# Kernel optimization log

Hardware: AMD Instinct MI355X
Metric: run time of the kernel (lower is better)

Reference implementation:

```python
import jax, jax.numpy as jnp
import numpy as np

COMMITMENT_COST = 0.25


def setup_inputs() -> dict:
    key = jax.random.key(0)
    k1, k2 = jax.random.split(key)
    x = jax.random.normal(k1, (32, 256, 32, 32), dtype=jnp.float32)
    codebook = jax.random.normal(k2, (1024, 256), dtype=jnp.float32) * 0.02
    return {"x": x, "codebook": codebook}


def reference(x, codebook):
    # x: [B, C, H, W] -> z: [B, H, W, C] (NHWC), C = embedding_dim
    B, C, H, W = x.shape
    z = jnp.transpose(x, (0, 2, 3, 1))
    zf = z.reshape(-1, C)  # [N, C], N = B*H*W
    # squared euclidean distance: ||z||^2 - 2 z.e + ||e||^2  -> [N, K]
    d = (
        jnp.sum(zf * zf, axis=-1, keepdims=True)
        - 2.0 * (zf @ codebook.T)
        + jnp.sum(codebook * codebook, axis=-1)
    )
    encoding_indices = jnp.argmin(d, axis=1)  # [N]
    quantized = codebook[encoding_indices].reshape(z.shape)  # [B, H, W, C]

    # training losses (entropy_loss_ratio == 0 -> entropy branch skipped)
    sg = jax.lax.stop_gradient
    e_latent_loss = jnp.mean((sg(quantized) - z) ** 2) * COMMITMENT_COST
    q_latent_loss = jnp.mean((quantized - sg(z)) ** 2)
    quantizer_loss = e_latent_loss + q_latent_loss

    # straight-through estimator
    quantized_st = z + sg(quantized - z)
    out = jnp.transpose(quantized_st, (0, 3, 1, 2))  # back to NCHW
    return out, quantizer_loss, e_latent_loss, q_latent_loss, encoding_indices
```

## Files before the change

### kernel.cpp

```cpp
#include <hip/hip_runtime.h>
#include <cfloat>

#define C_DIM   256
#define HW      1024
#define N_ROWS  32768
#define K_CODES 1024
#define ROWS    64
#define NCHUNK  32
#define WCHUNK_BYTES 8192
#define LISTCAP 128
#define DELTA   0.008f

#define OUT_ELEMS 8388608
#define LOSS_OFF  8388608
#define IDX_OFF   8388611

typedef _Float16 half8 __attribute__((ext_vector_type(8)));
typedef _Float16 f16x4 __attribute__((ext_vector_type(4)));
typedef float    f32x4 __attribute__((ext_vector_type(4)));

#define AS1 __attribute__((address_space(1)))
#define AS3 __attribute__((address_space(3)))

#define OFF_EBUF  0
#define OFF_EN    65536
#define OFF_S32   69632
#define OFF_M1W   69888
#define OFF_THR   70400
#define OFF_RES   70656
#define OFF_FIDX  71168
#define OFF_LCNT  71424
#define OFF_LMETA 71680
#define SMEM_BYTES 73728

#define QT_STRIDE 258

#define DPP_MIN(x, ctrl) fminf((x), __int_as_float(__builtin_amdgcn_update_dpp(0, __float_as_int(x), (ctrl), 0xf, 0xf, true)))

__global__ void prep_kernel(const float* __restrict__ cb, float* __restrict__ enorm,
                            char* __restrict__ cb16) {
    int k = blockIdx.x * 4 + (threadIdx.x >> 6);
    int lane = threadIdx.x & 63;
    float4 v = *(const float4*)(cb + k * C_DIM + lane * 4);
    double s = (double)v.x * v.x + (double)v.y * v.y + (double)v.z * v.z + (double)v.w * v.w;
    #pragma unroll
    for (int m = 1; m < 64; m <<= 1) s += __shfl_xor(s, m, 64);
    if (lane == 0) enorm[k] = (float)s;
    f16x4 h;
    h[0] = (_Float16)v.x; h[1] = (_Float16)v.y; h[2] = (_Float16)v.z; h[3] = (_Float16)v.w;
    int dst = ((k >> 5) << 14) + ((k & 31) << 9)
            + ((lane * 8) ^ ((k & 15) << 4) ^ ((k & 1) << 8));
    *(f16x4*)(cb16 + dst) = h;
}

__global__ __launch_bounds__(256, 2) void vq_main(
    const float* __restrict__ x, const float* __restrict__ cb,
    const float* __restrict__ enorm_g, const char* __restrict__ cb16,
    float* __restrict__ out, float* __restrict__ idx_out, float* __restrict__ t2_out)
{
    extern __shared__ char smem[];
    float* qt      = (float*)(smem + OFF_EBUF);
    float* en_lds  = (float*)(smem + OFF_EN);
    float* S32     = (float*)(smem + OFF_S32);
    float* m1w     = (float*)(smem + OFF_M1W);
    float* thr     = (float*)(smem + OFF_THR);
    unsigned long long* res = (unsigned long long*)(smem + OFF_RES);
    int*   fidx    = (int*)(smem + OFF_FIDX);
    int*   lcnt    = (int*)(smem + OFF_LCNT);
    unsigned int* lmeta = (unsigned int*)(smem + OFF_LMETA);

    const int t    = threadIdx.x;
    const int lane = t & 63;
    const int wv   = t >> 6;
    const int wr   = wv >> 1;
    const int wc   = wv & 1;
    const int l15  = lane & 15;
    const int l4   = lane >> 4;
    const int row0 = blockIdx.x * ROWS;
    const int b    = row0 >> 10;
    const int hw0  = row0 & 1023;
    const float* xb = x + b * (C_DIM * HW) + hw0;

    char* ebw = smem + OFF_EBUF + wv * (2 * WCHUNK_BYTES);
    const char* cbw = cb16 + (wc << 13);

    #pragma unroll
    for (int c2 = 0; c2 < 2; c2++) {
        const char* src = cbw + (c2 << 14);
        char* dst = ebw + c2 * WCHUNK_BYTES;
        #pragma unroll
        for (int i = 0; i < 8; i++) {
            __builtin_amdgcn_global_load_lds((const AS1 unsigned int*)(src + i * 1024 + lane * 16),
                                             (AS3 unsigned int*)(dst + i * 1024), 16, 0, 0);
        }
    }

    *(float4*)&en_lds[t * 4] = *(const float4*)(enorm_g + t * 4);
    if (t < 4) lcnt[t] = 0;

    half8 af[2][8];
    double s64[2] = {0.0, 0.0};
    #pragma unroll
    for (int rt = 0; rt < 2; rt++) {
        const float* xr = xb + wr * 32 + rt * 16 + l15;
        #pragma unroll
        for (int kk = 0; kk < 8; kk++) {
            float v[8];
            #pragma unroll
            for (int j = 0; j < 8; j++) v[j] = xr[(kk * 32 + l4 * 8 + j) * HW];
            #pragma unroll
            for (int j = 0; j < 8; j++) s64[rt] = fma((double)v[j], (double)v[j], s64[rt]);
            half8 h;
            #pragma unroll
            for (int j = 0; j < 8; j++) h[j] = (_Float16)(-2.0f * v[j]);
            af[rt][kk] = h;
        }
    }
    #pragma unroll
    for (int rt = 0; rt < 2; rt++) {
        s64[rt] += __shfl_xor(s64[rt], 16, 64);
        s64[rt] += __shfl_xor(s64[rt], 32, 64);
    }
    if (l4 == 0 && wc == 0) {
        S32[wr * 32 + l15]      = (float)s64[0];
        S32[wr * 32 + 16 + l15] = (float)s64[1];
    }
    __syncthreads();

    const int swzB = (l15 << 4) ^ ((l15 & 1) << 8);
    const int bofs = (l15 << 9);

    float s1v[2][4], s2v[2][4];
    int   c1v[2][4], c2v[2][4];
    #pragma unroll
    for (int rt = 0; rt < 2; rt++)
        #pragma unroll
        for (int r2 = 0; r2 < 4; r2++) {
            s1v[rt][r2] = FLT_MAX; s2v[rt][r2] = FLT_MAX;
            c1v[rt][r2] = 0;       c2v[rt][r2] = 0;
        }

    for (int ch = 0; ch < NCHUNK; ch++) {
        if (ch == NCHUNK - 1) { asm volatile("s_waitcnt vmcnt(0)" ::: "memory"); }
        else                  { asm volatile("s_waitcnt vmcnt(8)" ::: "memory"); }
        __builtin_amdgcn_sched_barrier(0);

        const char* ebc = ebw + (ch & 1) * WCHUNK_BYTES;
        half8 bf[8];
        #pragma unroll
        for (int kk = 0; kk < 8; kk++)
            bf[kk] = *(const half8*)(ebc + bofs + (((kk << 6) | (l4 << 4)) ^ swzB));
        asm volatile("s_waitcnt lgkmcnt(0)" ::: "memory");
        __builtin_amdgcn_sched_barrier(0);

        if (ch + 2 < NCHUNK) {
            const char* src = cbw + ((ch + 2) << 14);
            char* dst = ebw + (ch & 1) * WCHUNK_BYTES;
            #pragma unroll
            for (int i = 0; i < 8; i++) {
                __builtin_amdgcn_global_load_lds((const AS1 unsigned int*)(src + i * 1024 + lane * 16),
                                                 (AS3 unsigned int*)(dst + i * 1024), 16, 0, 0);
            }
        }

        const float en = en_lds[ch * 32 + wc * 16 + l15];
        f32x4 acc0 = {en, en, en, en};
        f32x4 acc1 = {en, en, en, en};
        #pragma unroll
        for (int kk = 0; kk < 8; kk++) {
            acc0 = __builtin_amdgcn_mfma_f32_16x16x32_f16(af[0][kk], bf[kk], acc0, 0, 0, 0);
            acc1 = __builtin_amdgcn_mfma_f32_16x16x32_f16(af[1][kk], bf[kk], acc1, 0, 0, 0);
        }
        #pragma unroll
        for (int r2 = 0; r2 < 4; r2++) {
            float s0 = acc0[r2];
            if (s0 < s1v[0][r2]) {
                s2v[0][r2] = s1v[0][r2]; c2v[0][r2] = c1v[0][r2];
                s1v[0][r2] = s0;         c1v[0][r2] = ch;
            } else if (s0 < s2v[0][r2]) {
                s2v[0][r2] = s0;         c2v[0][r2] = ch;
            }
            float s1 = acc1[r2];
            if (s1 < s1v[1][r2]) {
                s2v[1][r2] = s1v[1][r2]; c2v[1][r2] = c1v[1][r2];
                s1v[1][r2] = s1;         c1v[1][r2] = ch;
            } else if (s1 < s2v[1][r2]) {
                s2v[1][r2] = s1;         c2v[1][r2] = ch;
            }
        }
    }

    #pragma unroll
    for (int rt = 0; rt < 2; rt++) {
        #pragma unroll
        for (int r2 = 0; r2 < 4; r2++) {
            float m = s1v[rt][r2];
            m = DPP_MIN(m, 0xB1);
            m = DPP_MIN(m, 0x4E);
            m = DPP_MIN(m, 0x141);
            m = DPP_MIN(m, 0x140);
            if (l15 == 0) m1w[wc * 64 + wr * 32 + rt * 16 + l4 * 4 + r2] = m;
        }
    }
    __syncthreads();
    if (t < 64) {
        thr[t] = fminf(m1w[t], m1w[64 + t]) + DELTA;
        res[t] = ~0ull;
    }
    __syncthreads();

    #pragma unroll
    for (int rt = 0; rt < 2; rt++) {
        #pragma unroll
        for (int r2 = 0; r2 < 4; r2++) {
            int row_l = wr * 32 + rt * 16 + l4 * 4 + r2;
            float tr = thr[row_l];
            if (s1v[rt][r2] < tr) {
                int code = c1v[rt][r2] * 32 + wc * 16 + l15;
                int slot = atomicAdd(&lcnt[wv], 1);
                if (slot < LISTCAP)
                    lmeta[wv * LISTCAP + slot] = ((unsigned)row_l << 16) | (unsigned)code;
            }
            if (s2v[rt][r2] < tr) {
                int code = c2v[rt][r2] * 32 + wc * 16 + l15;
                int slot = atomicAdd(&lcnt[wv], 1);
                if (slot < LISTCAP)
                    lmeta[wv * LISTCAP + slot] = ((unsigned)row_l << 16) | (unsigned)code;
            }
        }
    }
    __syncthreads();

    {
        int n = lcnt[wv]; if (n > LISTCAP) n = LISTCAP;
        for (int base = 0; base < n; base += 4) {
            int it = base + l4;
            if (it < n) {
                unsigned meta = lmeta[wv * LISTCAP + it];
                int row  = (int)(meta >> 16);
                int code = (int)(meta & 1023u);
                const float* xr = xb + row;
                const float* er = cb + code * C_DIM;
                double acc = 0.0;
                #pragma unroll
                for (int s2 = 0; s2 < 16; s2++) {
                    int c = l15 + 16 * s2;
                    acc = fma((double)xr[(size_t)c * HW], (double)er[c], acc);
                }
                acc += __shfl_xor(acc, 1, 64);
                acc += __shfl_xor(acc, 2, 64);
                acc += __shfl_xor(acc, 4, 64);
                acc += __shfl_xor(acc, 8, 64);
                if (l15 == 0) {
                    float Mf = (float)acc;
                    float t2 = __fadd_rn(__fsub_rn(S32[row], __fmul_rn(2.0f, Mf)), en_lds[code]);
                    unsigned long long pk =
                        ((unsigned long long)__float_as_uint(t2) << 32) | (unsigned long long)(unsigned)code;
                    atomicMin(&res[row], pk);
                }
            }
        }
    }
    __syncthreads();

    if (t < 64) {
        unsigned long long v = res[t];
        int code = (int)(v & 1023u);
        fidx[t] = code;
        idx_out[row0 + t] = (float)code;
        t2_out[row0 + t] = __uint_as_float((unsigned)(v >> 32));
    }

    float* ob = out + b * (C_DIM * HW) + hw0;
    #pragma unroll
    for (int half = 0; half < 2; half++) {
        __syncthreads();
        for (int idx = t; idx < 32 * 64; idx += 256) {
            int r  = idx >> 6;
            int c4 = idx & 63;
            const float* er = cb + fidx[half * 32 + r] * C_DIM;
            *(float4*)&qt[r * QT_STRIDE + c4 * 4] = *(const float4*)(er + c4 * 4);
        }
        __syncthreads();
        int rr = t & 31;
        int cg = t >> 5;
        for (int cc = cg; cc < C_DIM; cc += 8) {
            ob[cc * HW + half * 32 + rr] = qt[rr * QT_STRIDE + cc];
        }
    }
}

__global__ void loss_kernel(const float* __restrict__ t2min, float* __restrict__ losses) {
    __shared__ double sh[256];
    int t = threadIdx.x;
    double a = 0.0;
    const int per = N_ROWS / 256;
    for (int i = t * per; i < t * per + per; i++) a += (double)t2min[i];
    sh[t] = a;
    __syncthreads();
    for (int s = 128; s > 0; s >>= 1) {
        if (t < s) sh[t] += sh[t + s];
        __syncthreads();
    }
    if (t == 0) {
        double M = sh[0] / (double)OUT_ELEMS;
        losses[0] = (float)(1.25 * M);
        losses[1] = (float)(0.25 * M);
        losses[2] = (float)(M);
    }
}

extern "C" void kernel_launch(void* const* d_in, const int* in_sizes, int n_in,
                              void* d_out, int out_size, void* d_ws, size_t ws_size,
                              hipStream_t stream) {
    const float* x  = (const float*)d_in[0];
    const float* cb = (const float*)d_in[1];
    float* out     = (float*)d_out;
    float* losses  = out + LOSS_OFF;
    float* idx_out = out + IDX_OFF;

    char*  cb16     = (char*)d_ws;
    float* t2ws     = (float*)((char*)d_ws + 524288);
    float* enorm_ws = (float*)((char*)d_ws + 524288 + 131072);

    hipFuncSetAttribute(reinterpret_cast<const void*>(vq_main),
                        hipFuncAttributeMaxDynamicSharedMemorySize, SMEM_BYTES);

    prep_kernel<<<K_CODES / 4, 256, 0, stream>>>(cb, enorm_ws, cb16);
    vq_main<<<N_ROWS / ROWS, 256, SMEM_BYTES, stream>>>(x, cb, enorm_ws, cb16, out, idx_out, t2ws);
    loss_kernel<<<1, 256, 0, stream>>>(t2ws, losses);
}
```

Measured before the change: 74.80 us.

## Halve rows per block and split codebook across four waves for occupancy

Each block now handles 32 rows instead of 64. All four waves share the same rows and each takes a different 16-code slice of every 64-code chunk, so there are 16 chunk iterations instead of 32. Per-wave LDS buffering drops from double to single buffering, which cuts shared memory roughly in half, and launch bounds move to 4 blocks per CU to raise occupancy and double the grid size. In exchange, each block reloads the x tile and codebook for fewer rows, so codebook traffic per row doubles. The prefetch also loses overlap, since each chunk waits on vmcnt(0) before it can compute.

New measurement: 157.3 us. 2.1x slower.

```diff
diff --git a/kernel.cpp b/kernel.cpp
--- a/kernel.cpp
+++ b/kernel.cpp
@@ -5,8 +5,8 @@
 #define HW      1024
 #define N_ROWS  32768
 #define K_CODES 1024
-#define ROWS    64
-#define NCHUNK  32
+#define ROWS    32
+#define NCHUNK  16
 #define WCHUNK_BYTES 8192
 #define LISTCAP 128
 #define DELTA   0.008f
@@ -23,15 +23,15 @@
 #define AS3 __attribute__((address_space(3)))
 
 #define OFF_EBUF  0
-#define OFF_EN    65536
-#define OFF_S32   69632
-#define OFF_M1W   69888
-#define OFF_THR   70400
-#define OFF_RES   70656
-#define OFF_FIDX  71168
-#define OFF_LCNT  71424
-#define OFF_LMETA 71680
-#define SMEM_BYTES 73728
+#define OFF_EN    32768
+#define OFF_S32   36864
+#define OFF_M1W   36992
+#define OFF_THR   37504
+#define OFF_RES   37632
+#define OFF_FIDX  37888
+#define OFF_LCNT  38016
+#define OFF_LMETA 38144
+#define SMEM_BYTES 40448
 
 #define QT_STRIDE 258
 
@@ -53,7 +53,7 @@
     *(f16x4*)(cb16 + dst) = h;
 }
 
-__global__ __launch_bounds__(256, 2) void vq_main(
+__global__ __launch_bounds__(256, 4) void vq_main(
     const float* __restrict__ x, const float* __restrict__ cb,
     const float* __restrict__ enorm_g, const char* __restrict__ cb16,
     float* __restrict__ out, float* __restrict__ idx_out, float* __restrict__ t2_out)
@@ -71,9 +71,7 @@
 
     const int t    = threadIdx.x;
     const int lane = t & 63;
-    const int wv   = t >> 6;
-    const int wr   = wv >> 1;
-    const int wc   = wv & 1;
+    const int wq   = t >> 6;
     const int l15  = lane & 15;
     const int l4   = lane >> 4;
     const int row0 = blockIdx.x * ROWS;
@@ -81,17 +79,14 @@
     const int hw0  = row0 & 1023;
     const float* xb = x + b * (C_DIM * HW) + hw0;
 
-    char* ebw = smem + OFF_EBUF + wv * (2 * WCHUNK_BYTES);
-    const char* cbw = cb16 + (wc << 13);
-
-    #pragma unroll
-    for (int c2 = 0; c2 < 2; c2++) {
-        const char* src = cbw + (c2 << 14);
-        char* dst = ebw + c2 * WCHUNK_BYTES;
+    char* ebw = smem + OFF_EBUF + wq * WCHUNK_BYTES;
+
+    {
+        const char* src = cb16 + wq * WCHUNK_BYTES;
         #pragma unroll
         for (int i = 0; i < 8; i++) {
             __builtin_amdgcn_global_load_lds((const AS1 unsigned int*)(src + i * 1024 + lane * 16),
-                                             (AS3 unsigned int*)(dst + i * 1024), 16, 0, 0);
+                                             (AS3 unsigned int*)(ebw + i * 1024), 16, 0, 0);
         }
     }
 
@@ -102,7 +97,7 @@
     double s64[2] = {0.0, 0.0};
     #pragma unroll
     for (int rt = 0; rt < 2; rt++) {
-        const float* xr = xb + wr * 32 + rt * 16 + l15;
+        const float* xr = xb + rt * 16 + l15;
         #pragma unroll
         for (int kk = 0; kk < 8; kk++) {
             float v[8];
@@ -121,9 +116,9 @@
         s64[rt] += __shfl_xor(s64[rt], 16, 64);
         s64[rt] += __shfl_xor(s64[rt], 32, 64);
     }
-    if (l4 == 0 && wc == 0) {
-        S32[wr * 32 + l15]      = (float)s64[0];
-        S32[wr * 32 + 16 + l15] = (float)s64[1];
+    if (wq == 0 && l4 == 0) {
+        S32[l15]      = (float)s64[0];
+        S32[16 + l15] = (float)s64[1];
     }
     __syncthreads();
 
@@ -141,29 +136,26 @@
         }
 
     for (int ch = 0; ch < NCHUNK; ch++) {
-        if (ch == NCHUNK - 1) { asm volatile("s_waitcnt vmcnt(0)" ::: "memory"); }
-        else                  { asm volatile("s_waitcnt vmcnt(8)" ::: "memory"); }
+        if (ch) { asm volatile("s_waitcnt vmcnt(0)" ::: "memory"); }
         __builtin_amdgcn_sched_barrier(0);
 
-        const char* ebc = ebw + (ch & 1) * WCHUNK_BYTES;
         half8 bf[8];
         #pragma unroll
         for (int kk = 0; kk < 8; kk++)
-            bf[kk] = *(const half8*)(ebc + bofs + (((kk << 6) | (l4 << 4)) ^ swzB));
+            bf[kk] = *(const half8*)(ebw + bofs + (((kk << 6) | (l4 << 4)) ^ swzB));
         asm volatile("s_waitcnt lgkmcnt(0)" ::: "memory");
         __builtin_amdgcn_sched_barrier(0);
 
-        if (ch + 2 < NCHUNK) {
-            const char* src = cbw + ((ch + 2) << 14);
-            char* dst = ebw + (ch & 1) * WCHUNK_BYTES;
+        if (ch + 1 < NCHUNK) {
+            const char* src = cb16 + (ch + 1) * 32768 + wq * WCHUNK_BYTES;
             #pragma unroll
             for (int i = 0; i < 8; i++) {
                 __builtin_amdgcn_global_load_lds((const AS1 unsigned int*)(src + i * 1024 + lane * 16),
-                                                 (AS3 unsigned int*)(dst + i * 1024), 16, 0, 0);
-            }
-        }
-
-        const float en = en_lds[ch * 32 + wc * 16 + l15];
+                                                 (AS3 unsigned int*)(ebw + i * 1024), 16, 0, 0);
+            }
+        }
+
+        const float en = en_lds[ch * 64 + wq * 16 + l15];
         f32x4 acc0 = {en, en, en, en};
         f32x4 acc1 = {en, en, en, en};
         #pragma unroll
@@ -199,12 +191,12 @@
             m = DPP_MIN(m, 0x4E);
             m = DPP_MIN(m, 0x141);
             m = DPP_MIN(m, 0x140);
-            if (l15 == 0) m1w[wc * 64 + wr * 32 + rt * 16 + l4 * 4 + r2] = m;
-        }
-    }
-    __syncthreads();
-    if (t < 64) {
-        thr[t] = fminf(m1w[t], m1w[64 + t]) + DELTA;
+            if (l15 == 0) m1w[wq * 32 + rt * 16 + l4 * 4 + r2] = m;
+        }
+    }
+    __syncthreads();
+    if (t < 32) {
+        thr[t] = fminf(fminf(m1w[t], m1w[32 + t]), fminf(m1w[64 + t], m1w[96 + t])) + DELTA;
         res[t] = ~0ull;
     }
     __syncthreads();
@@ -213,30 +205,30 @@
     for (int rt = 0; rt < 2; rt++) {
         #pragma unroll
         for (int r2 = 0; r2 < 4; r2++) {
-            int row_l = wr * 32 + rt * 16 + l4 * 4 + r2;
+            int row_l = rt * 16 + l4 * 4 + r2;
             float tr = thr[row_l];
             if (s1v[rt][r2] < tr) {
-                int code = c1v[rt][r2] * 32 + wc * 16 + l15;
-                int slot = atomicAdd(&lcnt[wv], 1);
+                int code = c1v[rt][r2] * 64 + wq * 16 + l15;
+                int slot = atomicAdd(&lcnt[wq], 1);
                 if (slot < LISTCAP)
-                    lmeta[wv * LISTCAP + slot] = ((unsigned)row_l << 16) | (unsigned)code;
+                    lmeta[wq * LISTCAP + slot] = ((unsigned)row_l << 16) | (unsigned)code;
             }
             if (s2v[rt][r2] < tr) {
-                int code = c2v[rt][r2] * 32 + wc * 16 + l15;
-                int slot = atomicAdd(&lcnt[wv], 1);
+                int code = c2v[rt][r2] * 64 + wq * 16 + l15;
+                int slot = atomicAdd(&lcnt[wq], 1);
                 if (slot < LISTCAP)
-                    lmeta[wv * LISTCAP + slot] = ((unsigned)row_l << 16) | (unsigned)code;
+                    lmeta[wq * LISTCAP + slot] = ((unsigned)row_l << 16) | (unsigned)code;
             }
         }
     }
     __syncthreads();
 
     {
-        int n = lcnt[wv]; if (n > LISTCAP) n = LISTCAP;
+        int n = lcnt[wq]; if (n > LISTCAP) n = LISTCAP;
         for (int base = 0; base < n; base += 4) {
             int it = base + l4;
             if (it < n) {
-                unsigned meta = lmeta[wv * LISTCAP + it];
+                unsigned meta = lmeta[wq * LISTCAP + it];
                 int row  = (int)(meta >> 16);
                 int code = (int)(meta & 1023u);
                 const float* xr = xb + row;
@@ -263,29 +255,28 @@
     }
     __syncthreads();
 
-    if (t < 64) {
+    if (t < 32) {
         unsigned long long v = res[t];
         int code = (int)(v & 1023u);
         fidx[t] = code;
         idx_out[row0 + t] = (float)code;
         t2_out[row0 + t] = __uint_as_float((unsigned)(v >> 32));
     }
-
-    float* ob = out + b * (C_DIM * HW) + hw0;
-    #pragma unroll
-    for (int half = 0; half < 2; half++) {
-        __syncthreads();
+    __syncthreads();
+
+    {
         for (int idx = t; idx < 32 * 64; idx += 256) {
             int r  = idx >> 6;
             int c4 = idx & 63;
-            const float* er = cb + fidx[half * 32 + r] * C_DIM;
+            const float* er = cb + fidx[r] * C_DIM;
             *(float4*)&qt[r * QT_STRIDE + c4 * 4] = *(const float4*)(er + c4 * 4);
         }
         __syncthreads();
+        float* ob = out + b * (C_DIM * HW) + hw0;
         int rr = t & 31;
         int cg = t >> 5;
         for (int cc = cg; cc < C_DIM; cc += 8) {
-            ob[cc * HW + half * 32 + rr] = qt[rr * QT_STRIDE + cc];
+            ob[cc * HW + rr] = qt[rr * QT_STRIDE + cc];
         }
     }
 }
```

## Pack chunk index into float low bits and use med3 top-2 tracking

Applied to the files above, without the earlier changes.

Replaces the branchy per-row top-2 tracker (scores plus chunk indices) with chunk ids packed into the low 5 mantissa bits of each score. fminf and fmed3 then keep the best two without branches or separate index registers. The fp16 codebook layout in global memory is also changed so each lane's B-fragment load is a plain linear offset instead of an XOR-swizzled address. Truncating the mantissa slightly perturbs scores, which the later refinement threshold with DELTA has to absorb, and the new layout may change LDS bank-conflict behaviour.

Result: faster. 69.95 us (-6.5%).

```diff
diff --git a/kernel.cpp b/kernel.cpp
--- a/kernel.cpp
+++ b/kernel.cpp
@@ -10,6 +10,7 @@
 #define WCHUNK_BYTES 8192
 #define LISTCAP 128
 #define DELTA   0.008f
+#define CMASK   0xFFFFFFE0u
 
 #define OUT_ELEMS 8388608
 #define LOSS_OFF  8388608
@@ -41,15 +42,16 @@
                             char* __restrict__ cb16) {
     int k = blockIdx.x * 4 + (threadIdx.x >> 6);
     int lane = threadIdx.x & 63;
-    float4 v = *(const float4*)(cb + k * C_DIM + lane * 4);
+    int c0 = lane * 4;
+    float4 v = *(const float4*)(cb + k * C_DIM + c0);
     double s = (double)v.x * v.x + (double)v.y * v.y + (double)v.z * v.z + (double)v.w * v.w;
     #pragma unroll
     for (int m = 1; m < 64; m <<= 1) s += __shfl_xor(s, m, 64);
     if (lane == 0) enorm[k] = (float)s;
     f16x4 h;
     h[0] = (_Float16)v.x; h[1] = (_Float16)v.y; h[2] = (_Float16)v.z; h[3] = (_Float16)v.w;
-    int dst = ((k >> 5) << 14) + ((k & 31) << 9)
-            + ((lane * 8) ^ ((k & 15) << 4) ^ ((k & 1) << 8));
+    int dst = ((k >> 4) << 13) + ((c0 >> 5) << 10) + (((c0 >> 3) & 3) << 8)
+            + ((k & 15) << 4) + ((c0 & 7) << 1);
     *(f16x4*)(cb16 + dst) = h;
 }
 
@@ -82,7 +84,7 @@
     const float* xb = x + b * (C_DIM * HW) + hw0;
 
     char* ebw = smem + OFF_EBUF + wv * (2 * WCHUNK_BYTES);
-    const char* cbw = cb16 + (wc << 13);
+    const char* cbw = cb16 + wc * WCHUNK_BYTES;
 
     #pragma unroll
     for (int c2 = 0; c2 < 2; c2++) {
@@ -127,18 +129,14 @@
     }
     __syncthreads();
 
-    const int swzB = (l15 << 4) ^ ((l15 & 1) << 8);
-    const int bofs = (l15 << 9);
-
-    float s1v[2][4], s2v[2][4];
-    int   c1v[2][4], c2v[2][4];
+    const int bbase  = (l4 << 8) + (l15 << 4);
+    const int enbase = wc * 16 + l15;
+
+    float u1[2][4], u2[2][4];
     #pragma unroll
     for (int rt = 0; rt < 2; rt++)
         #pragma unroll
-        for (int r2 = 0; r2 < 4; r2++) {
-            s1v[rt][r2] = FLT_MAX; s2v[rt][r2] = FLT_MAX;
-            c1v[rt][r2] = 0;       c2v[rt][r2] = 0;
-        }
+        for (int r2 = 0; r2 < 4; r2++) { u1[rt][r2] = FLT_MAX; u2[rt][r2] = FLT_MAX; }
 
     for (int ch = 0; ch < NCHUNK; ch++) {
         if (ch == NCHUNK - 1) { asm volatile("s_waitcnt vmcnt(0)" ::: "memory"); }
@@ -149,7 +147,7 @@
         half8 bf[8];
         #pragma unroll
         for (int kk = 0; kk < 8; kk++)
-            bf[kk] = *(const half8*)(ebc + bofs + (((kk << 6) | (l4 << 4)) ^ swzB));
+            bf[kk] = *(const half8*)(ebc + bbase + (kk << 10));
         asm volatile("s_waitcnt lgkmcnt(0)" ::: "memory");
         __builtin_amdgcn_sched_barrier(0);
 
@@ -163,7 +161,7 @@
             }
         }
 
-        const float en = en_lds[ch * 32 + wc * 16 + l15];
+        const float en = en_lds[enbase + ch * 32];
         f32x4 acc0 = {en, en, en, en};
         f32x4 acc1 = {en, en, en, en};
         #pragma unroll
@@ -173,20 +171,12 @@
         }
         #pragma unroll
         for (int r2 = 0; r2 < 4; r2++) {
-            float s0 = acc0[r2];
-            if (s0 < s1v[0][r2]) {
-                s2v[0][r2] = s1v[0][r2]; c2v[0][r2] = c1v[0][r2];
-                s1v[0][r2] = s0;         c1v[0][r2] = ch;
-            } else if (s0 < s2v[0][r2]) {
-                s2v[0][r2] = s0;         c2v[0][r2] = ch;
-            }
-            float s1 = acc1[r2];
-            if (s1 < s1v[1][r2]) {
-                s2v[1][r2] = s1v[1][r2]; c2v[1][r2] = c1v[1][r2];
-                s1v[1][r2] = s1;         c1v[1][r2] = ch;
-            } else if (s1 < s2v[1][r2]) {
-                s2v[1][r2] = s1;         c2v[1][r2] = ch;
-            }
+            float a0 = __uint_as_float((__float_as_uint(acc0[r2]) & CMASK) | (unsigned)ch);
+            u2[0][r2] = __builtin_amdgcn_fmed3f(a0, u1[0][r2], u2[0][r2]);
+            u1[0][r2] = fminf(u1[0][r2], a0);
+            float a1 = __uint_as_float((__float_as_uint(acc1[r2]) & CMASK) | (unsigned)ch);
+            u2[1][r2] = __builtin_amdgcn_fmed3f(a1, u1[1][r2], u2[1][r2]);
+            u1[1][r2] = fminf(u1[1][r2], a1);
         }
     }
 
@@ -194,7 +184,7 @@
     for (int rt = 0; rt < 2; rt++) {
         #pragma unroll
         for (int r2 = 0; r2 < 4; r2++) {
-            float m = s1v[rt][r2];
+            float m = u1[rt][r2];
             m = DPP_MIN(m, 0xB1);
             m = DPP_MIN(m, 0x4E);
             m = DPP_MIN(m, 0x141);
@@ -215,14 +205,16 @@
         for (int r2 = 0; r2 < 4; r2++) {
             int row_l = wr * 32 + rt * 16 + l4 * 4 + r2;
             float tr = thr[row_l];
-            if (s1v[rt][r2] < tr) {
-                int code = c1v[rt][r2] * 32 + wc * 16 + l15;
+            if (u1[rt][r2] < tr) {
+                int ch1 = (int)(__float_as_uint(u1[rt][r2]) & 31u);
+                int code = ch1 * 32 + wc * 16 + l15;
                 int slot = atomicAdd(&lcnt[wv], 1);
                 if (slot < LISTCAP)
                     lmeta[wv * LISTCAP + slot] = ((unsigned)row_l << 16) | (unsigned)code;
             }
-            if (s2v[rt][r2] < tr) {
-                int code = c2v[rt][r2] * 32 + wc * 16 + l15;
+            if (u2[rt][r2] < tr) {
+                int ch2 = (int)(__float_as_uint(u2[rt][r2]) & 31u);
+                int code = ch2 * 32 + wc * 16 + l15;
                 int slot = atomicAdd(&lcnt[wv], 1);
                 if (slot < LISTCAP)
                     lmeta[wv * LISTCAP + slot] = ((unsigned)row_l << 16) | (unsigned)code;
```
